# Optimization experiments

Hardware: AMD Instinct MI355X
Metric: run time of the kernel (lower is better)

## Reference

```python
import jax, jax.numpy as jnp
import numpy as np

B = 128                      # num_graphs (cell lines per batch)
SIZES = [706, 512, 256, 128] # nodes per graph at each level; final_node = 128
DIM = 256                    # dim_cell
DEG = 8                      # avg degree of gene-gene network
EPS = 1e-5                   # BatchNorm eps


def _build_graph():
    """Build per-graph edges (incl. self-loops, as GATConv adds) and predefined
    cluster assignments per layer, coarsening edges exactly like PyG max_pool
    (remove self-loops + coalesce). Replicated across B graphs with offsets."""
    rng = np.random.default_rng(0)
    e = rng.integers(0, SIZES[0], size=(2, SIZES[0] * DEG))
    e = e[:, e[0] != e[1]]
    e = np.unique(e, axis=1)
    edges, clusters = [], []
    cur = e
    for i in range(3):
        n_cur, n_next = SIZES[i], SIZES[i + 1]
        sl = np.arange(n_cur)
        e_sl = np.concatenate([cur, np.stack([sl, sl])], axis=1)  # add self-loops
        off = np.arange(B) * n_cur
        eg = (e_sl[:, None, :] + off[None, :, None]).reshape(2, -1)
        edges.append(eg.astype(np.int32))
        cl = np.concatenate([np.arange(n_next), rng.integers(0, n_next, size=n_cur - n_next)])
        rng.shuffle(cl)  # surjective cluster assignment n_cur -> n_next
        clg = (cl[None, :] + (np.arange(B) * n_next)[:, None]).reshape(-1)
        clusters.append(clg.astype(np.int32))
        src, dst = cl[cur[0]], cl[cur[1]]
        m = src != dst                      # pool_edge: remove self-loops
        cur = np.unique(np.stack([src[m], dst[m]]), axis=1)  # coalesce
    return edges, clusters


def setup_inputs() -> dict:
    edges, clusters = _build_graph()
    key = jax.random.key(0)
    ks = jax.random.split(key, 16)
    d = {"x": jax.random.normal(ks[0], (B * SIZES[0], 3), jnp.float32)}
    ins = [3, DIM, DIM]
    for i in range(3):
        s = 1.0 / np.sqrt(ins[i])
        a = 1.0 / np.sqrt(DIM)
        d[f"W{i}"] = jax.random.normal(ks[1 + i], (ins[i], DIM), jnp.float32) * s
        d[f"asrc{i}"] = jax.random.normal(ks[4 + i], (DIM,), jnp.float32) * a
        d[f"adst{i}"] = jax.random.normal(ks[7 + i], (DIM,), jnp.float32) * a
        d[f"b{i}"] = jnp.zeros((DIM,), jnp.float32)
        d[f"edge{i}"] = jnp.asarray(edges[i])
        d[f"cluster{i}"] = jnp.asarray(clusters[i])
    return d


def _gat(x, edge, W, a_s, a_d, b):
    """PyG GATConv, heads=1, negative_slope=0.2 (self-loops pre-added in edge)."""
    N = x.shape[0]
    h = x @ W                                    # [N, D]
    src, dst = edge[0], edge[1]
    e = jax.nn.leaky_relu((h * a_s).sum(-1)[src] + (h * a_d).sum(-1)[dst], 0.2)
    m = jax.ops.segment_max(e, dst, num_segments=N)     # segment softmax (stable)
    ex = jnp.exp(e - m[dst])
    ssum = jax.ops.segment_sum(ex, dst, num_segments=N)
    alpha = ex / ssum[dst]
    out = jax.ops.segment_sum(h[src] * alpha[:, None], dst, num_segments=N)
    return out + b


def _forward(x, Ws, a_ss, a_ds, bs, edges, clusters):
    for i in range(3):
        x = jax.nn.relu(_gat(x, edges[i], Ws[i], a_ss[i], a_ds[i], bs[i]))
        # max_pool: scatter-max over predefined clusters (coarsen nodes)
        x = jax.ops.segment_max(x, clusters[i], num_segments=B * SIZES[i + 1])
        # BatchNorm1d(affine=False), training mode: biased batch stats
        mean = x.mean(0)
        var = x.var(0)
        x = (x - mean) * jax.lax.rsqrt(var + EPS)
    return x.reshape(B, SIZES[3] * DIM)


def reference(x, W0, W1, W2, asrc0, asrc1, asrc2, adst0, adst1, adst2,
              b0, b1, b2, edge0, edge1, edge2, cluster0, cluster1, cluster2):
    return _forward(x, (W0, W1, W2), (asrc0, asrc1, asrc2), (adst0, adst1, adst2),
                    (b0, b1, b2), (edge0, edge1, edge2), (cluster0, cluster1, cluster2))
```

## Files before the change

### kernel.cpp

```cpp
#include <hip/hip_runtime.h>
#include <hip/hip_fp16.h>

#define DIM 256
#define MAXMEM 16
#define MAXDEG 288
#define NSH 16

typedef _Float16 f16x8 __attribute__((ext_vector_type(8)));
typedef float f32x4 __attribute__((ext_vector_type(4)));

__device__ inline unsigned short f2h(float f) {
  return __half_as_ushort(__float2half_rn(f));
}
__device__ inline float h2f(unsigned short u) {
  return __half2float(__ushort_as_half(u));
}
__device__ inline __half2 hmax2_(__half2 a, __half2 b) {
  __half2 c;
  c.x = __hgt(a.x, b.x) ? a.x : b.x;
  c.y = __hgt(a.y, b.y) ? a.y : b.y;
  return c;
}


struct BktArgs {
  const int* esrc[3]; const int* edst[3]; const int* cl[3];
  int Eb[3]; int Nb[3]; int est[3];
  int* bdeg[3]; int* bccnt[3]; int* bebkt[3]; int* bcbkt[3];
};

__global__ __launch_bounds__(256) void l0_bucket(
    const float* __restrict__ x, const float* __restrict__ W,
    const float* __restrict__ asv, const float* __restrict__ adv,
    unsigned short* __restrict__ h, float* __restrict__ ssrc,
    float* __restrict__ sdst, int N, int Nb0, int l0Blocks, int bgx,
    BktArgs a) {
  if ((int)blockIdx.x >= l0Blocks) {
    int bb = blockIdx.x - l0Blocks;
    int L = bb / bgx;
    int i = (bb % bgx) * 256 + threadIdx.x;
    if (i < a.Eb[L]) {
      int d = a.edst[L][i];
      int slot = atomicAdd(&a.bdeg[L][d], 1);
      if (slot < a.est[L]) a.bebkt[L][d * a.est[L] + slot] = a.esrc[L][i];
    }
    if (i < a.Nb[L]) {
      int c = a.cl[L][i];
      int slot = atomicAdd(&a.bccnt[L][c], 1);
      if (slot < MAXMEM) a.bcbkt[L][c * MAXMEM + slot] = i;
    }
    return;
  }
  int wid = (blockIdx.x * 256 + threadIdx.x) >> 6;
  int lane = threadIdx.x & 63;
  if (wid >= N) return;
  int nb = wid >> 7, g = wid & 127;
  const float* xr = x + ((size_t)g * Nb0 + nb) * 3;
  float x0 = xr[0], x1 = xr[1], x2 = xr[2];
  int c = lane * 4;
  float4 w0 = *(const float4*)(W + c);
  float4 w1 = *(const float4*)(W + 256 + c);
  float4 w2 = *(const float4*)(W + 512 + c);
  float4 hv;
  hv.x = fmaf(x0, w0.x, fmaf(x1, w1.x, x2 * w2.x));
  hv.y = fmaf(x0, w0.y, fmaf(x1, w1.y, x2 * w2.y));
  hv.z = fmaf(x0, w0.z, fmaf(x1, w1.z, x2 * w2.z));
  hv.w = fmaf(x0, w0.w, fmaf(x1, w1.w, x2 * w2.w));
  ((ushort4*)(h + (size_t)wid * DIM))[lane] =
      make_ushort4(f2h(hv.x), f2h(hv.y), f2h(hv.z), f2h(hv.w));
  float4 a1 = ((const float4*)asv)[lane];
  float4 a2 = ((const float4*)adv)[lane];
  float d1 = hv.x * a1.x + hv.y * a1.y + hv.z * a1.z + hv.w * a1.w;
  float d2 = hv.x * a2.x + hv.y * a2.y + hv.z * a2.z + hv.w * a2.w;
  for (int o = 32; o > 0; o >>= 1) {
    d1 += __shfl_down(d1, o);
    d2 += __shfl_down(d2, o);
  }
  if (lane == 0) { ssrc[wid] = d1; sdst[wid] = d2; }
}

__global__ __launch_bounds__(256) void prep_k(
    const float* __restrict__ W, const float* __restrict__ stats,
    float invN, unsigned short* __restrict__ Wt, float* __restrict__ cvec) {
  int n = blockIdx.x;
  int k = threadIdx.x;
  float s = 0.f, q = 0.f;
#pragma unroll
  for (int sh = 0; sh < NSH; sh++) {
    s += stats[sh * 512 + k];
    q += stats[sh * 512 + 256 + k];
  }
  float mu = s * invN;
  float var = q * invN - mu * mu;
  float istd = rsqrtf(var + 1e-5f);
  float w = W[(size_t)k * 256 + n] * istd;
  Wt[(size_t)n * 256 + k] = f2h(w);
  __shared__ float red[256];
  red[k] = mu * w;
  __syncthreads();
  for (int sft = 128; sft > 0; sft >>= 1) {
    if (k < sft) red[k] += red[k + sft];
    __syncthreads();
  }
  if (k == 0) cvec[n] = -red[0];
}

__global__ __launch_bounds__(256) void gemm_mfma(
    const unsigned short* __restrict__ A, const unsigned short* __restrict__ Wt,
    const float* __restrict__ cvec, const float* __restrict__ asv,
    const float* __restrict__ adv, unsigned short* __restrict__ H,
    float* __restrict__ ssrc, float* __restrict__ sdst, int M) {
  __shared__ unsigned short Bs[256 * 128];
  int tid = threadIdx.x;
  int wave = tid >> 6, lane = tid & 63;
  int m0 = blockIdx.x * 128 + wave * 32;
  int row = lane & 15, quad = lane >> 4;
  int swz = (row & 7) << 3;

  const unsigned short* Ap = A + (size_t)(m0 + row) * 256 + quad * 8;
  f32x4 acc[2][16] = {};

#pragma unroll
  for (int kh = 0; kh < 2; kh++) {
    if (kh) __syncthreads();
#pragma unroll
    for (int k = 0; k < 16; k++) {
      int c = k * 256 + tid;
      f16x8 v = *(const f16x8*)(const void*)(Wt + (size_t)(c >> 4) * 256 +
                                             kh * 128 + (c & 15) * 8);
      *(f16x8*)(void*)(&Bs[(c * 8) ^ (((c >> 4) & 7) << 3)]) = v;
    }
    __syncthreads();
#pragma unroll
    for (int j2 = 0; j2 < 4; j2++) {
      int j = kh * 4 + j2;
      f16x8 a0 = *(const f16x8*)(const void*)(Ap + j * 32);
      f16x8 a1 = *(const f16x8*)(const void*)(Ap + 16 * 256 + j * 32);
#pragma unroll
      for (int nt = 0; nt < 16; nt++) {
        f16x8 b = *(const f16x8*)(const void*)(
            &Bs[((nt * 16 + row) * 128 + j2 * 32 + quad * 8) ^ swz]);
        acc[0][nt] = __builtin_amdgcn_mfma_f32_16x16x32_f16(a0, b, acc[0][nt], 0, 0, 0);
        acc[1][nt] = __builtin_amdgcn_mfma_f32_16x16x32_f16(a1, b, acc[1][nt], 0, 0, 0);
      }
    }
  }

  float sav[16], sdv[16], cv[16];
#pragma unroll
  for (int nt = 0; nt < 16; nt++) {
    sav[nt] = asv[nt * 16 + row];
    sdv[nt] = adv[nt * 16 + row];
    cv[nt] = cvec[nt * 16 + row];
  }
#pragma unroll
  for (int sub = 0; sub < 2; sub++)
#pragma unroll
    for (int r = 0; r < 4; r++) {
      int mm = m0 + sub * 16 + quad * 4 + r;
      unsigned short* out = H + (size_t)mm * 256 + row;
      float d1 = 0.f, d2 = 0.f;
#pragma unroll
      for (int nt = 0; nt < 16; nt++) {
        float hv = acc[sub][nt][r] + cv[nt];
        out[nt * 16] = f2h(hv);
        d1 = fmaf(hv, sav[nt], d1);
        d2 = fmaf(hv, sdv[nt], d2);
      }
      for (int o = 1; o < 16; o <<= 1) {
        d1 += __shfl_xor(d1, o);
        d2 += __shfl_xor(d2, o);
      }
      if (row == 0) { ssrc[mm] = d1; sdst[mm] = d2; }
    }
}

__global__ __launch_bounds__(256) void gat_fused(
    const unsigned short* __restrict__ h, const int* __restrict__ bdeg,
    const int* __restrict__ bebkt, int estride,
    const int* __restrict__ bccnt, const int* __restrict__ bcbkt,
    const float* __restrict__ ssrc, const float* __restrict__ sdst,
    const float* __restrict__ bias, unsigned short* __restrict__ pooled,
    int Mb, int lgMb) {
  __shared__ float pLDS[2][MAXDEG * 8];
  __shared__ float psumW[2][32];
  int b = blockIdx.x;
  int x = b & 7, t = b >> 3;
  int c = t & (Mb - 1);
  int set = x + 8 * (t >> lgMb);
  int tid = threadIdx.x;
  int wave = tid >> 6, lane = tid & 63;
  int gl = tid >> 5;
  int ch = tid & 31;
  int g = set * 8 + gl;
  int nm = bccnt[c]; if (nm > MAXMEM) nm = MAXMEM;
  float4 bf0 = *(const float4*)(bias + ch * 8);
  float4 bf1 = *(const float4*)(bias + ch * 8 + 4);
  __half2 hb[4] = {__floats2half2_rn(bf0.x, bf0.y), __floats2half2_rn(bf0.z, bf0.w),
                   __floats2half2_rn(bf1.x, bf1.y), __floats2half2_rn(bf1.z, bf1.w)};
  __half2 z = __float2half2_rn(0.f);
  __half2 best[4] = {z, z, z, z};

  auto score = [&](int bi, int nb, int deg) {
    float part = 0.f;
    const int* bk = bebkt + nb * estride;
    for (int jj = tid; jj < deg * 8; jj += 256) {
      int j = jj >> 3, gi = jj & 7;
      int s = bk[j];
      float tt = ssrc[s * 128 + set * 8 + gi] + sdst[nb * 128 + set * 8 + gi];
      tt = tt > 0.f ? tt : 0.2f * tt;
      float p = __expf(tt);
      pLDS[bi][jj] = p;
      part += p;
    }
    part += __shfl_xor(part, 8);
    part += __shfl_xor(part, 16);
    part += __shfl_xor(part, 32);
    if (lane < 8) psumW[bi][wave * 8 + lane] = part;
  };

  int nbC = 0, degC = 0;
  if (nm > 0) {
    nbC = __builtin_amdgcn_readfirstlane(bcbkt[c * MAXMEM]);
    degC = __builtin_amdgcn_readfirstlane(bdeg[nbC]);
    if (degC > estride) degC = estride;
    score(0, nbC, degC);
  }
  for (int mi = 0; mi < nm; mi++) {
    __syncthreads();
    int nbN = 0, degN = 0;
    if (mi + 1 < nm) {
      nbN = __builtin_amdgcn_readfirstlane(bcbkt[c * MAXMEM + mi + 1]);
      degN = __builtin_amdgcn_readfirstlane(bdeg[nbN]);
      if (degN > estride) degN = estride;
      score((mi + 1) & 1, nbN, degN);
    }
    int bi = mi & 1;
    const float* pl = pLDS[bi];
    float inv = 1.f / (psumW[bi][gl] + psumW[bi][8 + gl] +
                       psumW[bi][16 + gl] + psumW[bi][24 + gl]);
    const int* bk = bebkt + nbC * estride;
    __half2 acc[4] = {z, z, z, z};
    int j = 0;
    for (; j + 4 <= degC; j += 4) {
      int4 ss = *(const int4*)(bk + j);
      __half2 hq0 = __float2half2_rn(pl[(j + 0) * 8 + gl] * inv);
      __half2 hq1 = __float2half2_rn(pl[(j + 1) * 8 + gl] * inv);
      __half2 hq2 = __float2half2_rn(pl[(j + 2) * 8 + gl] * inv);
      __half2 hq3 = __float2half2_rn(pl[(j + 3) * 8 + gl] * inv);
      uint4 v0 = *(const uint4*)(h + ((size_t)ss.x * 128 + g) * DIM + ch * 8);
      uint4 v1 = *(const uint4*)(h + ((size_t)ss.y * 128 + g) * DIM + ch * 8);
      uint4 v2 = *(const uint4*)(h + ((size_t)ss.z * 128 + g) * DIM + ch * 8);
      uint4 v3 = *(const uint4*)(h + ((size_t)ss.w * 128 + g) * DIM + ch * 8);
      union { uint4 u; __half2 p[4]; } u0, u1, u2, u3;
      u0.u = v0; u1.u = v1; u2.u = v2; u3.u = v3;
#pragma unroll
      for (int i = 0; i < 4; i++) {
        acc[i] = __hfma2(u0.p[i], hq0, acc[i]);
        acc[i] = __hfma2(u1.p[i], hq1, acc[i]);
        acc[i] = __hfma2(u2.p[i], hq2, acc[i]);
        acc[i] = __hfma2(u3.p[i], hq3, acc[i]);
      }
    }
    for (; j < degC; j++) {
      int s = bk[j];
      __half2 hq = __float2half2_rn(pl[j * 8 + gl] * inv);
      uint4 v0 = *(const uint4*)(h + ((size_t)s * 128 + g) * DIM + ch * 8);
      union { uint4 u; __half2 p[4]; } u0; u0.u = v0;
#pragma unroll
      for (int i = 0; i < 4; i++) acc[i] = __hfma2(u0.p[i], hq, acc[i]);
    }
#pragma unroll
    for (int i = 0; i < 4; i++)
      best[i] = hmax2_(best[i], __hadd2(acc[i], hb[i]));
    nbC = nbN; degC = degN;
  }
  union { uint4 u; __half2 p[4]; } o;
#pragma unroll
  for (int i = 0; i < 4; i++) o.p[i] = best[i];
  *(uint4*)(pooled + ((size_t)c * 128 + g) * DIM + ch * 8) = o.u;
}

__global__ __launch_bounds__(256) void stats_k(
    const unsigned short* __restrict__ x, float* __restrict__ statL, int M) {
  int tid = threadIdx.x;
  int ch = tid & 31;
  int rg = tid >> 5;
  float s[8] = {}, q[8] = {};
  for (int r = blockIdx.x * 8 + rg; r < M; r += gridDim.x * 8) {
    uint4 v = *(const uint4*)(x + (size_t)r * DIM + ch * 8);
    union { uint4 u; __half2 p[4]; } uu; uu.u = v;
#pragma unroll
    for (int i = 0; i < 4; i++) {
      float2 f = __half22float2(uu.p[i]);
      s[2 * i]     += f.x; q[2 * i]     = fmaf(f.x, f.x, q[2 * i]);
      s[2 * i + 1] += f.y; q[2 * i + 1] = fmaf(f.y, f.y, q[2 * i + 1]);
    }
  }
  __shared__ float sm[512];
  sm[tid] = 0.f; sm[tid + 256] = 0.f;
  __syncthreads();
#pragma unroll
  for (int i = 0; i < 8; i++) {
    atomicAdd(&sm[ch * 8 + i], s[i]);
    atomicAdd(&sm[256 + ch * 8 + i], q[i]);
  }
  __syncthreads();
  float* sg = statL + (blockIdx.x & (NSH - 1)) * 512;
  atomicAdd(&sg[tid], sm[tid]);
  atomicAdd(&sg[tid + 256], sm[tid + 256]);
}

__global__ void norm_out(const unsigned short* __restrict__ xin,
                         float* __restrict__ xout,
                         const float* __restrict__ stats,
                         float invN, int Mb, int total) {
  int idx = blockIdx.x * 256 + threadIdx.x;
  if (idx >= total) return;
  int ch = idx & 255;
  int r = idx >> 8;
  int g = r & 127, c = r >> 7;
  float s = 0.f, q = 0.f;
#pragma unroll
  for (int sh = 0; sh < NSH; sh++) {
    s += stats[sh * 512 + ch];
    q += stats[sh * 512 + 256 + ch];
  }
  float mu = s * invN;
  float var = q * invN - mu * mu;
  float v = (h2f(xin[idx]) - mu) * rsqrtf(var + 1e-5f);
  xout[((size_t)g * Mb + c) * 256 + ch] = v;
}

extern "C" void kernel_launch(void* const* d_in, const int* in_sizes, int n_in,
                              void* d_out, int out_size, void* d_ws, size_t ws_size,
                              hipStream_t stream) {
  const int B = 128;
  const int Nb[4] = {706, 512, 256, 128};
  const int Ns[4] = {128 * 706, 128 * 512, 128 * 256, 128 * 128};
  const int lgMb[3] = {9, 8, 7};
  const int EST[3] = {64, 160, 288};

  int iW[3], iA[3], iD[3], iB_[3], iE[3], iC[3];
  if (in_sizes[2] == 256) {
    for (int i = 0; i < 3; i++) {
      iW[i] = 1 + 6 * i; iA[i] = 2 + 6 * i; iD[i] = 3 + 6 * i;
      iB_[i] = 4 + 6 * i; iE[i] = 5 + 6 * i; iC[i] = 6 + 6 * i;
    }
  } else {
    for (int i = 0; i < 3; i++) {
      iW[i] = 1 + i; iA[i] = 4 + i; iD[i] = 7 + i;
      iB_[i] = 10 + i; iE[i] = 13 + i; iC[i] = 16 + i;
    }
  }
  int E[3];
  for (int i = 0; i < 3; i++) E[i] = in_sizes[iE[i]] / 2;

  int bebktOff[3], bcbktOff[3];
  size_t bebktTot = 0, bcbktTot = 0;
  for (int i = 0; i < 3; i++) {
    bebktOff[i] = (int)bebktTot; bebktTot += (size_t)Nb[i] * EST[i];
    bcbktOff[i] = (int)bcbktTot; bcbktTot += (size_t)Nb[i + 1] * MAXMEM;
  }

  char* wsp = (char*)d_ws;
  size_t o = 0;
  auto alloc = [&](size_t bytes) -> void* {
    void* p = wsp + o;
    o = (o + bytes + 255) & ~(size_t)255;
    return p;
  };
  unsigned short* h      = (unsigned short*)alloc((size_t)Ns[0] * DIM * 2);
  unsigned short* pooled = (unsigned short*)alloc((size_t)Ns[1] * DIM * 2);
  float* ssrc   = (float*)alloc((size_t)Ns[0] * 4);
  float* sdst   = (float*)alloc((size_t)Ns[0] * 4);
  float* statbuf= (float*)alloc((size_t)3 * NSH * 512 * 4);
  int*   bmeta  = (int*)alloc((size_t)3 * (Nb[0] + Nb[1]) * 4);
  char*  zend   = wsp + o;
  int*   bebkt  = (int*)alloc(bebktTot * 4);
  int*   bcbkt  = (int*)alloc(bcbktTot * 4);
  unsigned short* Wt = (unsigned short*)alloc(256 * 256 * 2);
  float* cvec   = (float*)alloc(256 * 4);
  (void)ws_size; (void)n_in; (void)out_size;

  const float* xin = (const float*)d_in[0];

  hipMemsetAsync(statbuf, 0, (size_t)(zend - (char*)statbuf), stream);

  BktArgs ba;
  int maxG = 0;
  for (int L = 0; L < 3; L++) {
    int Eb = E[L] / B;
    ba.esrc[L] = (const int*)d_in[iE[L]];
    ba.edst[L] = ba.esrc[L] + E[L];
    ba.cl[L]   = (const int*)d_in[iC[L]];
    ba.Eb[L] = Eb; ba.Nb[L] = Nb[L]; ba.est[L] = EST[L];
    ba.bdeg[L]  = bmeta + L * (Nb[0] + Nb[1]);
    ba.bccnt[L] = ba.bdeg[L] + Nb[L];
    ba.bebkt[L] = bebkt + bebktOff[L];
    ba.bcbkt[L] = bcbkt + bcbktOff[L];
    int gneed = (Eb > Nb[L] ? Eb : Nb[L]);
    if (gneed > maxG) maxG = gneed;
  }
  int bgx = (maxG + 255) / 256;

  for (int L = 0; L < 3; L++) {
    int N = Ns[L], M = Ns[L + 1];
    int NbL = Nb[L];
    const float* W  = (const float*)d_in[iW[L]];
    const float* av = (const float*)d_in[iA[L]];
    const float* dv = (const float*)d_in[iD[L]];
    const float* bv = (const float*)d_in[iB_[L]];
    float* statL = statbuf + (size_t)L * NSH * 512;
    int* bdeg = bmeta + L * (Nb[0] + Nb[1]);
    int* bccnt = bdeg + NbL;
    int* beb = bebkt + bebktOff[L];
    int* bcb = bcbkt + bcbktOff[L];

    if (L == 0) {
      int l0Blocks = (N + 3) / 4;
      l0_bucket<<<l0Blocks + bgx * 3, 256, 0, stream>>>(
          xin, W, av, dv, h, ssrc, sdst, N, NbL, l0Blocks, bgx, ba);
    } else {
      float* pstat = statbuf + (size_t)(L - 1) * NSH * 512;
      prep_k<<<256, 256, 0, stream>>>(W, pstat, 1.0f / (float)N, Wt, cvec);
      gemm_mfma<<<N / 128, 256, 0, stream>>>(pooled, Wt, cvec, av, dv,
                                             h, ssrc, sdst, N);
    }

    int MbL = Nb[L + 1];
    gat_fused<<<MbL * 16, 256, 0, stream>>>(h, bdeg, beb, EST[L], bccnt, bcb,
                                            ssrc, sdst, bv, pooled,
                                            MbL, lgMb[L]);

    stats_k<<<512, 256, 0, stream>>>(pooled, statL, M);
  }

  norm_out<<<((size_t)Ns[3] * DIM + 255) / 256, 256, 0, stream>>>(
      pooled, (float*)d_out, statbuf + (size_t)2 * NSH * 512,
      1.0f / (float)Ns[3], Nb[3], Ns[3] * DIM);
}
```

Baseline: 318.2 us.

## Double-buffer GEMM weight tiles in LDS using direct global-to-LDS loads

The GEMM kernel now splits the weight matrix into four K-quarters and stages them into two LDS buffers with global_load_lds, so the next quarter is fetched while MFMAs run on the current one. This replaces the earlier two-phase load-then-compute scheme, which went through registers and stalled at each barrier. The LDS footprint stays the same. The swizzle is now applied to the source addresses so the async copies land in a bank-conflict-avoiding layout, which adds indexing complexity and depends on the lane-to-LDS-address mapping of global_load_lds.

```diff
diff --git a/kernel.cpp b/kernel.cpp
--- a/kernel.cpp
+++ b/kernel.cpp
@@ -110,7 +110,7 @@
     const float* __restrict__ cvec, const float* __restrict__ asv,
     const float* __restrict__ adv, unsigned short* __restrict__ H,
     float* __restrict__ ssrc, float* __restrict__ sdst, int M) {
-  __shared__ unsigned short Bs[256 * 128];
+  __shared__ unsigned short Bq[2][256 * 64];
   int tid = threadIdx.x;
   int wave = tid >> 6, lane = tid & 63;
   int m0 = blockIdx.x * 128 + wave * 32;
@@ -120,30 +120,45 @@
   const unsigned short* Ap = A + (size_t)(m0 + row) * 256 + quad * 8;
   f32x4 acc[2][16] = {};
 
-#pragma unroll
-  for (int kh = 0; kh < 2; kh++) {
-    if (kh) __syncthreads();
-#pragma unroll
-    for (int k = 0; k < 16; k++) {
-      int c = k * 256 + tid;
-      f16x8 v = *(const f16x8*)(const void*)(Wt + (size_t)(c >> 4) * 256 +
-                                             kh * 128 + (c & 15) * 8);
-      *(f16x8*)(void*)(&Bs[(c * 8) ^ (((c >> 4) & 7) << 3)]) = v;
+  auto stage = [&](int bi, int q) {
+#pragma unroll
+    for (int k = 0; k < 8; k++) {
+      int m = k * 256 + tid;
+      int col = m >> 3;
+      int sub = (m & 7) ^ (col & 7);
+      const unsigned short* src = Wt + (size_t)col * 256 + q * 64 + sub * 8;
+      unsigned short* dst = &Bq[bi][(size_t)(k * 256 + wave * 64) * 8];
+      __builtin_amdgcn_global_load_lds(
+          (const __attribute__((address_space(1))) unsigned int*)src,
+          (__attribute__((address_space(3))) unsigned int*)dst, 16, 0, 0);
+    }
+  };
+
+  stage(0, 0);
+  __syncthreads();
+#pragma unroll
+  for (int q = 0; q < 4; q++) {
+    int bi = q & 1;
+    f16x8 a00 = *(const f16x8*)(const void*)(Ap + (q * 2 + 0) * 32);
+    f16x8 a10 = *(const f16x8*)(const void*)(Ap + 16 * 256 + (q * 2 + 0) * 32);
+    f16x8 a01 = *(const f16x8*)(const void*)(Ap + (q * 2 + 1) * 32);
+    f16x8 a11 = *(const f16x8*)(const void*)(Ap + 16 * 256 + (q * 2 + 1) * 32);
+    if (q < 3) stage(bi ^ 1, q + 1);
+#pragma unroll
+    for (int nt = 0; nt < 16; nt++) {
+      f16x8 b = *(const f16x8*)(const void*)(
+          &Bq[bi][((nt * 16 + row) * 64 + quad * 8) ^ swz]);
+      acc[0][nt] = __builtin_amdgcn_mfma_f32_16x16x32_f16(a00, b, acc[0][nt], 0, 0, 0);
+      acc[1][nt] = __builtin_amdgcn_mfma_f32_16x16x32_f16(a10, b, acc[1][nt], 0, 0, 0);
+    }
+#pragma unroll
+    for (int nt = 0; nt < 16; nt++) {
+      f16x8 b = *(const f16x8*)(const void*)(
+          &Bq[bi][((nt * 16 + row) * 64 + 32 + quad * 8) ^ swz]);
+      acc[0][nt] = __builtin_amdgcn_mfma_f32_16x16x32_f16(a01, b, acc[0][nt], 0, 0, 0);
+      acc[1][nt] = __builtin_amdgcn_mfma_f32_16x16x32_f16(a11, b, acc[1][nt], 0, 0, 0);
     }
     __syncthreads();
-#pragma unroll
-    for (int j2 = 0; j2 < 4; j2++) {
-      int j = kh * 4 + j2;
-      f16x8 a0 = *(const f16x8*)(const void*)(Ap + j * 32);
-      f16x8 a1 = *(const f16x8*)(const void*)(Ap + 16 * 256 + j * 32);
-#pragma unroll
-      for (int nt = 0; nt < 16; nt++) {
-        f16x8 b = *(const f16x8*)(const void*)(
-            &Bs[((nt * 16 + row) * 128 + j2 * 32 + quad * 8) ^ swz]);
-        acc[0][nt] = __builtin_amdgcn_mfma_f32_16x16x32_f16(a0, b, acc[0][nt], 0, 0, 0);
-        acc[1][nt] = __builtin_amdgcn_mfma_f32_16x16x32_f16(a1, b, acc[1][nt], 0, 0, 0);
-      }
-    }
   }
 
   float sav[16], sdv[16], cv[16];
```

Result: no change. 314.8 us, median of 2 (-1.1%).
